# Kernel tuning notes

Hardware: AMD Instinct MI355X
Metric: run time of the kernel (lower is better)

## Reference

```python
import jax, jax.numpy as jnp
import numpy as np

B, T, D, H = 512, 1024, 64, 64     # batch, time, input_size, hidden_size
R = 4                              # number of reward heads
MH = 32                            # MLP hidden size


def setup_inputs() -> dict:
    key = jax.random.key(0)
    ks = jax.random.split(key, 16)
    s = lambda k, shape, scale=1.0: jax.random.normal(k, shape, dtype=jnp.float32) * scale
    inp = {
        "x": s(ks[0], (B, T, D)),
        # learned initial states (nn.Parameter randn(1,1,H) -> store as (H,))
        "h_init": s(ks[1], (H,)),
        "c_init": s(ks[2], (H,)),
        # LSTM params, PyTorch layout: W_ih (4H, D), W_hh (4H, H), gate order i,f,g,o
        "W_ih": s(ks[3], (4 * H, D), 1.0 / np.sqrt(H)),
        "W_hh": s(ks[4], (4 * H, H), 1.0 / np.sqrt(H)),
        "b_ih": s(ks[5], (4 * H,), 1.0 / np.sqrt(H)),
        "b_hh": s(ks[6], (4 * H,), 1.0 / np.sqrt(H)),
        # R stacked MLP heads: Linear(H,MH) -> ReLU -> Linear(MH,MH) -> ReLU -> Linear(MH,1)
        "W1": s(ks[7], (R, MH, H), 1.0 / np.sqrt(H)),
        "b1": s(ks[8], (R, MH), 1.0 / np.sqrt(H)),
        "W2": s(ks[9], (R, MH, MH), 1.0 / np.sqrt(MH)),
        "b2": s(ks[10], (R, MH), 1.0 / np.sqrt(MH)),
        "W3": s(ks[11], (R, 1, MH), 1.0 / np.sqrt(MH)),
        "b3": s(ks[12], (R, 1), 1.0 / np.sqrt(MH)),
    }
    return inp


def _lstm(x, h0, c0, W_ih, W_hh, b_ih, b_hh):
    # x: (B, T, D). Returns y: (B, T, H).
    Hh = h0.shape[-1]
    b = b_ih + b_hh                      # (4H,)
    # precompute input projections for all steps: (T, B, 4H)
    xg = jnp.einsum('btd,gd->tbg', x, W_ih) + b

    def step(carry, xg_t):
        h, c = carry                     # (B, H) each
        gates = xg_t + h @ W_hh.T        # (B, 4H)
        i, f, g, o = jnp.split(gates, 4, axis=-1)
        c = jax.nn.sigmoid(f) * c + jax.nn.sigmoid(i) * jnp.tanh(g)
        h = jax.nn.sigmoid(o) * jnp.tanh(c)
        return (h, c), h

    Bb = x.shape[0]
    h0b = jnp.broadcast_to(h0, (Bb, Hh))
    c0b = jnp.broadcast_to(c0, (Bb, Hh))
    _, ys = jax.lax.scan(step, (h0b, c0b), xg)   # ys: (T, B, H)
    return jnp.transpose(ys, (1, 0, 2))


def _heads(y, W1, b1, W2, b2, W3, b3):
    # y: (B, T, H) -> (R, B, T); all R heads computed in one batched einsum chain
    h1 = jax.nn.relu(jnp.einsum('bth,rmh->rbtm', y, W1) + b1[:, None, None, :])
    h2 = jax.nn.relu(jnp.einsum('rbtm,rnm->rbtn', h1, W2) + b2[:, None, None, :])
    out = jnp.einsum('rbtn,ron->rbto', h2, W3) + b3[:, None, None, :]
    return out[..., 0]                   # squeeze last dim -> (R, B, T)


def reference(x, h_init, c_init, W_ih, W_hh, b_ih, b_hh, W1, b1, W2, b2, W3, b3):
    y = _lstm(x, h_init, c_init, W_ih, W_hh, b_ih, b_hh)
    outs = _heads(y, W1, b1, W2, b2, W3, b3)   # (R, B, T); row r == rewards[r] head
    return (y, outs)
```

## Files before the change

kernel.cpp:

```cpp
#include <hip/hip_runtime.h>

#define BB 512
#define TT 1024
#define DD 64
#define HH 64
#define G4 256
#define RR 4
#define MHH 32
#define BT (BB * TT)
#define Y_SIZE (BB * TT * HH)

typedef _Float16 half8 __attribute__((ext_vector_type(8)));
typedef _Float16 half4 __attribute__((ext_vector_type(4)));
typedef float f32x4 __attribute__((ext_vector_type(4)));

#define MFMA16(a, b, c) __builtin_amdgcn_mfma_f32_16x16x32_f16((a), (b), (c), 0, 0, 0)

__device__ __forceinline__ float sigm(float x) {
    return __builtin_amdgcn_rcpf(1.0f + __expf(-x));
}
__device__ __forceinline__ float tanh_(float x) {
    return 1.0f - 2.0f * __builtin_amdgcn_rcpf(1.0f + __expf(2.0f * x));
}

__device__ __forceinline__ half8 cvt8(f32x4 a, f32x4 b) {
    half8 h;
    h[0] = (_Float16)a[0]; h[1] = (_Float16)a[1];
    h[2] = (_Float16)a[2]; h[3] = (_Float16)a[3];
    h[4] = (_Float16)b[0]; h[5] = (_Float16)b[1];
    h[6] = (_Float16)b[2]; h[7] = (_Float16)b[3];
    return h;
}

__global__ __launch_bounds__(256) void lstm_kernel(
    const float* __restrict__ x, const float* __restrict__ h_init,
    const float* __restrict__ c_init, const float* __restrict__ W_ih,
    const float* __restrict__ W_hh, const float* __restrict__ b_ih,
    const float* __restrict__ b_hh, float* __restrict__ y)
{
    __shared__ alignas(16) _Float16 xch[2][16][2][DD];
    __shared__ alignas(16) _Float16 hst[2][2][HH];

    const int tid  = threadIdx.x;
    const int wave = tid >> 6;
    const int lane = tid & 63;
    const int col  = lane & 15;
    const int quad = lane >> 4;
    const int sel  = (lane >> 3) & 1;
    const int r_act = lane >> 5;
    const int j    = (wave << 4) + col;
    const bool writer = ((lane >> 4) & 1) == 0;

    const int b0 = blockIdx.x * 2;

    half8 bf[4][4];
    float bias[4];
#pragma unroll
    for (int G = 0; G < 4; ++G) {
        const int n = (G << 6) + j;
        bias[G] = b_ih[n] + b_hh[n];
#pragma unroll
        for (int c = 0; c < 4; ++c) {
            const float* src = (c < 2) ? (W_ih + n * DD + c * 32 + quad * 8)
                                       : (W_hh + n * HH + (c - 2) * 32 + quad * 8);
            f32x4 w0 = *(const f32x4*)src;
            f32x4 w1 = *(const f32x4*)(src + 4);
            bf[G][c] = cvt8(w0, w1);
        }
    }

    float c_state = c_init[j];

    if (tid < 128) {
        const int rr = tid >> 6, jj = tid & 63;
        hst[0][rr][jj] = (_Float16)h_init[jj];
    }
    {
        const int ss = tid >> 4, rr = (tid >> 3) & 1, j0 = (tid & 7) << 3;
        const float* src = x + ((b0 + rr) * TT + ss) * DD + j0;
        f32x4 g0 = *(const f32x4*)src;
        f32x4 g1 = *(const f32x4*)(src + 4);
        *(half8*)&xch[0][ss][rr][j0] = cvt8(g0, g1);
    }
    __syncthreads();

    const int ss_pf = tid >> 4, rr_pf = (tid >> 3) & 1, j0_pf = (tid & 7) << 3;

    for (int ci = 0; ci < 64; ++ci) {
        const int buf = ci & 1;
        const bool pf = (ci + 1) < 64;
        f32x4 g0, g1;
        if (pf) {
            const float* src = x + ((b0 + rr_pf) * TT + ((ci + 1) << 4) + ss_pf) * DD + j0_pf;
            g0 = *(const f32x4*)src;
            g1 = *(const f32x4*)(src + 4);
        }
#pragma unroll
        for (int s = 0; s < 16; ++s) {
            const int t = (ci << 4) + s;
            const int p = s & 1;
            const _Float16* xrow = &xch[buf][s][sel][0];
            half8 a0 = *(const half8*)(xrow + quad * 8);
            half8 a1 = *(const half8*)(xrow + 32 + quad * 8);
            const _Float16* hrow = &hst[p][sel][0];
            half8 a2 = *(const half8*)(hrow + quad * 8);
            half8 a3 = *(const half8*)(hrow + 32 + quad * 8);

            f32x4 acc0 = {bias[0], bias[0], bias[0], bias[0]};
            f32x4 acc1 = {bias[1], bias[1], bias[1], bias[1]};
            f32x4 acc2 = {bias[2], bias[2], bias[2], bias[2]};
            f32x4 acc3 = {bias[3], bias[3], bias[3], bias[3]};
            acc0 = MFMA16(a0, bf[0][0], acc0); acc0 = MFMA16(a1, bf[0][1], acc0);
            acc0 = MFMA16(a2, bf[0][2], acc0); acc0 = MFMA16(a3, bf[0][3], acc0);
            acc1 = MFMA16(a0, bf[1][0], acc1); acc1 = MFMA16(a1, bf[1][1], acc1);
            acc1 = MFMA16(a2, bf[1][2], acc1); acc1 = MFMA16(a3, bf[1][3], acc1);
            acc2 = MFMA16(a0, bf[2][0], acc2); acc2 = MFMA16(a1, bf[2][1], acc2);
            acc2 = MFMA16(a2, bf[2][2], acc2); acc2 = MFMA16(a3, bf[2][3], acc2);
            acc3 = MFMA16(a0, bf[3][0], acc3); acc3 = MFMA16(a1, bf[3][1], acc3);
            acc3 = MFMA16(a2, bf[3][2], acc3); acc3 = MFMA16(a3, bf[3][3], acc3);

            const float si = sigm(acc0[0]);
            const float sf = sigm(acc1[0]);
            const float tg = tanh_(acc2[0]);
            const float so = sigm(acc3[0]);
            c_state = sf * c_state + si * tg;
            const float hv = so * tanh_(c_state);
            if (writer) {
                hst[p ^ 1][r_act][j] = (_Float16)hv;
                y[((b0 + r_act) * TT + t) * HH + j] = hv;
            }
            if (s == 15 && pf) {
                *(half8*)&xch[buf ^ 1][ss_pf][rr_pf][j0_pf] = cvt8(g0, g1);
            }
            __syncthreads();
        }
    }
}

__global__ __launch_bounds__(256) void heads_kernel(
    const float* __restrict__ y,
    const float* __restrict__ W1, const float* __restrict__ b1,
    const float* __restrict__ W2, const float* __restrict__ b2,
    const float* __restrict__ W3, const float* __restrict__ b3,
    float* __restrict__ outs)
{
    __shared__ alignas(16) _Float16 ybuf[64][72];
    __shared__ alignas(16) _Float16 h1buf[64][136];
    __shared__ alignas(16) _Float16 h2buf[64][136];

    const int tid  = threadIdx.x;
    const int wave = tid >> 6;
    const int lane = tid & 63;
    const int col  = lane & 15;
    const int quad = lane >> 4;
    const int arow = (wave << 4) + col;

    half8 w1f[8][2]; float bias1[8];
#pragma unroll
    for (int nt = 0; nt < 8; ++nt) {
        const int n = nt * 16 + col;
        bias1[nt] = b1[n];
#pragma unroll
        for (int c = 0; c < 2; ++c) {
            const float* src = W1 + n * 64 + c * 32 + quad * 8;
            w1f[nt][c] = cvt8(*(const f32x4*)src, *(const f32x4*)(src + 4));
        }
    }
    half8 w2f[8]; float bias2[8];
#pragma unroll
    for (int nt = 0; nt < 8; ++nt) {
        const int n = nt * 16 + col;
        bias2[nt] = b2[n];
        const float* src = W2 + n * 32 + quad * 8;
        w2f[nt] = cvt8(*(const f32x4*)src, *(const f32x4*)(src + 4));
    }
    const int hd3 = tid >> 6, row3 = tid & 63;
    float w3r[32];
#pragma unroll
    for (int i = 0; i < 32; i += 4) {
        f32x4 v = *(const f32x4*)(W3 + hd3 * 32 + i);
        w3r[i] = v[0]; w3r[i + 1] = v[1]; w3r[i + 2] = v[2]; w3r[i + 3] = v[3];
    }
    const float b3v = b3[hd3];

    for (int st = 0; st < 4; ++st) {
        const long base_row = (long)blockIdx.x * 256 + st * 64;
#pragma unroll
        for (int jj = 0; jj < 4; ++jj) {
            const int off = (jj * 256 + tid) * 4;
            const int row = off >> 6, cc = off & 63;
            f32x4 v = *(const f32x4*)(y + base_row * 64 + off);
            half4 hv = {(_Float16)v[0], (_Float16)v[1], (_Float16)v[2], (_Float16)v[3]};
            *(half4*)&ybuf[row][cc] = hv;
        }
        __syncthreads();

        half8 a0 = *(const half8*)&ybuf[arow][quad * 8];
        half8 a1 = *(const half8*)&ybuf[arow][32 + quad * 8];
#pragma unroll
        for (int nt = 0; nt < 8; ++nt) {
            f32x4 acc = {bias1[nt], bias1[nt], bias1[nt], bias1[nt]};
            acc = MFMA16(a0, w1f[nt][0], acc);
            acc = MFMA16(a1, w1f[nt][1], acc);
#pragma unroll
            for (int r = 0; r < 4; ++r) {
                float v = acc[r] > 0.0f ? acc[r] : 0.0f;
                h1buf[(wave << 4) + (quad << 2) + r][nt * 16 + col] = (_Float16)v;
            }
        }
        __syncthreads();

        half8 ah[4];
#pragma unroll
        for (int hd = 0; hd < 4; ++hd)
            ah[hd] = *(const half8*)&h1buf[arow][hd * 32 + quad * 8];
#pragma unroll
        for (int nt = 0; nt < 8; ++nt) {
            f32x4 acc = {bias2[nt], bias2[nt], bias2[nt], bias2[nt]};
            acc = MFMA16(ah[nt >> 1], w2f[nt], acc);
#pragma unroll
            for (int r = 0; r < 4; ++r) {
                float v = acc[r] > 0.0f ? acc[r] : 0.0f;
                h2buf[(wave << 4) + (quad << 2) + r][nt * 16 + col] = (_Float16)v;
            }
        }
        __syncthreads();

        float acc = b3v;
#pragma unroll
        for (int c = 0; c < 4; ++c) {
            half8 v = *(const half8*)&h2buf[row3][hd3 * 32 + c * 8];
#pragma unroll
            for (int u = 0; u < 8; ++u)
                acc = fmaf((float)v[u], w3r[c * 8 + u], acc);
        }
        outs[(long)hd3 * BT + base_row + row3] = acc;
        __syncthreads();
    }
}

extern "C" void kernel_launch(void* const* d_in, const int* in_sizes, int n_in,
                              void* d_out, int out_size, void* d_ws, size_t ws_size,
                              hipStream_t stream) {
    (void)in_sizes; (void)n_in; (void)out_size; (void)d_ws; (void)ws_size;
    const float* x      = (const float*)d_in[0];
    const float* h_init = (const float*)d_in[1];
    const float* c_init = (const float*)d_in[2];
    const float* W_ih   = (const float*)d_in[3];
    const float* W_hh   = (const float*)d_in[4];
    const float* b_ih   = (const float*)d_in[5];
    const float* b_hh   = (const float*)d_in[6];
    const float* W1     = (const float*)d_in[7];
    const float* b1     = (const float*)d_in[8];
    const float* W2     = (const float*)d_in[9];
    const float* b2     = (const float*)d_in[10];
    const float* W3     = (const float*)d_in[11];
    const float* b3     = (const float*)d_in[12];
    float* y    = (float*)d_out;
    float* outs = y + Y_SIZE;

    lstm_kernel<<<dim3(256), dim3(256), 0, stream>>>(x, h_init, c_init, W_ih, W_hh,
                                                     b_ih, b_hh, y);
    heads_kernel<<<dim3(2048), dim3(256), 0, stream>>>(y, W1, b1, W2, b2, W3, b3, outs);
}
```

Baseline: 570.5 us.

## Fuse MLP reward heads into LSTM kernel per 16-step chunk

The separate heads kernel is removed and its three MLP layers run inside the LSTM kernel after each 16-timestep chunk. Each chunk's hidden states are staged in shared memory, written to y with coalesced vector stores, and fed straight to MFMA head computation. This avoids re-reading y from global memory and a second launch. The cost is extra work on the serial recurrence path for each chunk. The x prefetch for the next chunk also moves from being in flight during the chunk to a synchronous load at the chunk boundary, which may expose load latency.

```diff
diff --git a/kernel.cpp b/kernel.cpp
--- a/kernel.cpp
+++ b/kernel.cpp
@@ -4,14 +4,12 @@
 #define TT 1024
 #define DD 64
 #define HH 64
-#define G4 256
 #define RR 4
 #define MHH 32
 #define BT (BB * TT)
 #define Y_SIZE (BB * TT * HH)
 
 typedef _Float16 half8 __attribute__((ext_vector_type(8)));
-typedef _Float16 half4 __attribute__((ext_vector_type(4)));
 typedef float f32x4 __attribute__((ext_vector_type(4)));
 
 #define MFMA16(a, b, c) __builtin_amdgcn_mfma_f32_16x16x32_f16((a), (b), (c), 0, 0, 0)
@@ -22,7 +20,6 @@
 __device__ __forceinline__ float tanh_(float x) {
     return 1.0f - 2.0f * __builtin_amdgcn_rcpf(1.0f + __expf(2.0f * x));
 }
-
 __device__ __forceinline__ half8 cvt8(f32x4 a, f32x4 b) {
     half8 h;
     h[0] = (_Float16)a[0]; h[1] = (_Float16)a[1];
@@ -32,14 +29,22 @@
     return h;
 }
 
-__global__ __launch_bounds__(256) void lstm_kernel(
+__global__ __launch_bounds__(256) void lstm_fused_kernel(
     const float* __restrict__ x, const float* __restrict__ h_init,
     const float* __restrict__ c_init, const float* __restrict__ W_ih,
     const float* __restrict__ W_hh, const float* __restrict__ b_ih,
-    const float* __restrict__ b_hh, float* __restrict__ y)
+    const float* __restrict__ b_hh,
+    const float* __restrict__ W1, const float* __restrict__ b1,
+    const float* __restrict__ W2, const float* __restrict__ b2,
+    const float* __restrict__ W3, const float* __restrict__ b3,
+    float* __restrict__ y, float* __restrict__ outs)
 {
     __shared__ alignas(16) _Float16 xch[2][16][2][DD];
     __shared__ alignas(16) _Float16 hst[2][2][HH];
+    __shared__ alignas(16) float    ybuf[2][16][68];
+    __shared__ alignas(16) _Float16 h1b[4][16][72];
+    __shared__ alignas(16) _Float16 h2b[4][16][72];
+    __shared__ alignas(16) float    w3s[128];
 
     const int tid  = threadIdx.x;
     const int wave = tid >> 6;
@@ -63,11 +68,36 @@
         for (int c = 0; c < 4; ++c) {
             const float* src = (c < 2) ? (W_ih + n * DD + c * 32 + quad * 8)
                                        : (W_hh + n * HH + (c - 2) * 32 + quad * 8);
-            f32x4 w0 = *(const f32x4*)src;
-            f32x4 w1 = *(const f32x4*)(src + 4);
-            bf[G][c] = cvt8(w0, w1);
-        }
-    }
+            bf[G][c] = cvt8(*(const f32x4*)src, *(const f32x4*)(src + 4));
+        }
+    }
+
+    const int pair = wave >> 1;
+    const int r_h  = wave & 1;
+    half8 w1f[4][2]; float bias1[4];
+#pragma unroll
+    for (int i = 0; i < 4; ++i) {
+        const int n1 = pair * 64 + i * 16 + col;
+        bias1[i] = b1[n1];
+#pragma unroll
+        for (int c = 0; c < 2; ++c) {
+            const float* src = W1 + n1 * 64 + c * 32 + quad * 8;
+            w1f[i][c] = cvt8(*(const f32x4*)src, *(const f32x4*)(src + 4));
+        }
+    }
+    half8 w2f[2][2]; float bias2[2][2];
+#pragma unroll
+    for (int hl = 0; hl < 2; ++hl)
+#pragma unroll
+        for (int i2 = 0; i2 < 2; ++i2) {
+            const int n2 = (pair * 2 + hl) * 32 + i2 * 16 + col;
+            bias2[hl][i2] = b2[n2];
+            const float* src = W2 + n2 * 32 + quad * 8;
+            w2f[hl][i2] = cvt8(*(const f32x4*)src, *(const f32x4*)(src + 4));
+        }
+    if (tid < 128) w3s[tid] = W3[tid];
+    const int g_l3 = pair * 2 + ((lane >> 4) & 1);
+    const float b3v = b3[g_l3];
 
     float c_state = c_init[j];
 
@@ -75,36 +105,25 @@
         const int rr = tid >> 6, jj = tid & 63;
         hst[0][rr][jj] = (_Float16)h_init[jj];
     }
+    const int ss_ld = tid >> 4, rr_ld = (tid >> 3) & 1, j0_ld = (tid & 7) << 3;
     {
-        const int ss = tid >> 4, rr = (tid >> 3) & 1, j0 = (tid & 7) << 3;
-        const float* src = x + ((b0 + rr) * TT + ss) * DD + j0;
-        f32x4 g0 = *(const f32x4*)src;
-        f32x4 g1 = *(const f32x4*)(src + 4);
-        *(half8*)&xch[0][ss][rr][j0] = cvt8(g0, g1);
+        const float* src = x + ((b0 + rr_ld) * TT + ss_ld) * DD + j0_ld;
+        *(half8*)&xch[0][ss_ld][rr_ld][j0_ld] =
+            cvt8(*(const f32x4*)src, *(const f32x4*)(src + 4));
     }
     __syncthreads();
-
-    const int ss_pf = tid >> 4, rr_pf = (tid >> 3) & 1, j0_pf = (tid & 7) << 3;
 
     for (int ci = 0; ci < 64; ++ci) {
         const int buf = ci & 1;
-        const bool pf = (ci + 1) < 64;
-        f32x4 g0, g1;
-        if (pf) {
-            const float* src = x + ((b0 + rr_pf) * TT + ((ci + 1) << 4) + ss_pf) * DD + j0_pf;
-            g0 = *(const f32x4*)src;
-            g1 = *(const f32x4*)(src + 4);
-        }
 #pragma unroll
         for (int s = 0; s < 16; ++s) {
-            const int t = (ci << 4) + s;
             const int p = s & 1;
+            const _Float16* hrow = &hst[p][sel][0];
+            half8 a2 = *(const half8*)(hrow + quad * 8);
+            half8 a3 = *(const half8*)(hrow + 32 + quad * 8);
             const _Float16* xrow = &xch[buf][s][sel][0];
             half8 a0 = *(const half8*)(xrow + quad * 8);
             half8 a1 = *(const half8*)(xrow + 32 + quad * 8);
-            const _Float16* hrow = &hst[p][sel][0];
-            half8 a2 = *(const half8*)(hrow + quad * 8);
-            half8 a3 = *(const half8*)(hrow + 32 + quad * 8);
 
             f32x4 acc0 = {bias[0], bias[0], bias[0], bias[0]};
             f32x4 acc1 = {bias[1], bias[1], bias[1], bias[1]};
@@ -127,114 +146,81 @@
             const float hv = so * tanh_(c_state);
             if (writer) {
                 hst[p ^ 1][r_act][j] = (_Float16)hv;
-                y[((b0 + r_act) * TT + t) * HH + j] = hv;
-            }
-            if (s == 15 && pf) {
-                *(half8*)&xch[buf ^ 1][ss_pf][rr_pf][j0_pf] = cvt8(g0, g1);
+                ybuf[r_act][s][j] = hv;
             }
             __syncthreads();
         }
-    }
-}
-
-__global__ __launch_bounds__(256) void heads_kernel(
-    const float* __restrict__ y,
-    const float* __restrict__ W1, const float* __restrict__ b1,
-    const float* __restrict__ W2, const float* __restrict__ b2,
-    const float* __restrict__ W3, const float* __restrict__ b3,
-    float* __restrict__ outs)
-{
-    __shared__ alignas(16) _Float16 ybuf[64][72];
-    __shared__ alignas(16) _Float16 h1buf[64][136];
-    __shared__ alignas(16) _Float16 h2buf[64][136];
-
-    const int tid  = threadIdx.x;
-    const int wave = tid >> 6;
-    const int lane = tid & 63;
-    const int col  = lane & 15;
-    const int quad = lane >> 4;
-    const int arow = (wave << 4) + col;
-
-    half8 w1f[8][2]; float bias1[8];
-#pragma unroll
-    for (int nt = 0; nt < 8; ++nt) {
-        const int n = nt * 16 + col;
-        bias1[nt] = b1[n];
-#pragma unroll
-        for (int c = 0; c < 2; ++c) {
-            const float* src = W1 + n * 64 + c * 32 + quad * 8;
-            w1f[nt][c] = cvt8(*(const f32x4*)src, *(const f32x4*)(src + 4));
-        }
-    }
-    half8 w2f[8]; float bias2[8];
-#pragma unroll
-    for (int nt = 0; nt < 8; ++nt) {
-        const int n = nt * 16 + col;
-        bias2[nt] = b2[n];
-        const float* src = W2 + n * 32 + quad * 8;
-        w2f[nt] = cvt8(*(const f32x4*)src, *(const f32x4*)(src + 4));
-    }
-    const int hd3 = tid >> 6, row3 = tid & 63;
-    float w3r[32];
-#pragma unroll
-    for (int i = 0; i < 32; i += 4) {
-        f32x4 v = *(const f32x4*)(W3 + hd3 * 32 + i);
-        w3r[i] = v[0]; w3r[i + 1] = v[1]; w3r[i + 2] = v[2]; w3r[i + 3] = v[3];
-    }
-    const float b3v = b3[hd3];
-
-    for (int st = 0; st < 4; ++st) {
-        const long base_row = (long)blockIdx.x * 256 + st * 64;
-#pragma unroll
-        for (int jj = 0; jj < 4; ++jj) {
-            const int off = (jj * 256 + tid) * 4;
-            const int row = off >> 6, cc = off & 63;
-            f32x4 v = *(const f32x4*)(y + base_row * 64 + off);
-            half4 hv = {(_Float16)v[0], (_Float16)v[1], (_Float16)v[2], (_Float16)v[3]};
-            *(half4*)&ybuf[row][cc] = hv;
-        }
-        __syncthreads();
-
-        half8 a0 = *(const half8*)&ybuf[arow][quad * 8];
-        half8 a1 = *(const half8*)&ybuf[arow][32 + quad * 8];
-#pragma unroll
-        for (int nt = 0; nt < 8; ++nt) {
-            f32x4 acc = {bias1[nt], bias1[nt], bias1[nt], bias1[nt]};
-            acc = MFMA16(a0, w1f[nt][0], acc);
-            acc = MFMA16(a1, w1f[nt][1], acc);
-#pragma unroll
-            for (int r = 0; r < 4; ++r) {
-                float v = acc[r] > 0.0f ? acc[r] : 0.0f;
-                h1buf[(wave << 4) + (quad << 2) + r][nt * 16 + col] = (_Float16)v;
+
+        {
+            const int r = tid >> 7, s = (tid >> 3) & 15, j0 = (tid & 7) << 3;
+            f32x4 v0 = *(const f32x4*)&ybuf[r][s][j0];
+            f32x4 v1 = *(const f32x4*)&ybuf[r][s][j0 + 4];
+            float* dst = y + (((long)(b0 + r) * TT + (ci << 4) + s) << 6) + j0;
+            *(f32x4*)dst = v0;
+            *(f32x4*)(dst + 4) = v1;
+        }
+        if (ci + 1 < 64) {
+            const float* src =
+                x + ((b0 + rr_ld) * TT + ((ci + 1) << 4) + ss_ld) * DD + j0_ld;
+            *(half8*)&xch[buf ^ 1][ss_ld][rr_ld][j0_ld] =
+                cvt8(*(const f32x4*)src, *(const f32x4*)(src + 4));
+        }
+        {
+            const int sr = lane & 15;
+            const float* yb = &ybuf[r_h][sr][0];
+            half8 a0 = cvt8(*(const f32x4*)(yb + quad * 8),
+                            *(const f32x4*)(yb + quad * 8 + 4));
+            half8 a1 = cvt8(*(const f32x4*)(yb + 32 + quad * 8),
+                            *(const f32x4*)(yb + 32 + quad * 8 + 4));
+#pragma unroll
+            for (int i = 0; i < 4; ++i) {
+                f32x4 acc = {bias1[i], bias1[i], bias1[i], bias1[i]};
+                acc = MFMA16(a0, w1f[i][0], acc);
+                acc = MFMA16(a1, w1f[i][1], acc);
+#pragma unroll
+                for (int r = 0; r < 4; ++r) {
+                    float v = acc[r] > 0.0f ? acc[r] : 0.0f;
+                    h1b[wave][(quad << 2) + r][i * 16 + col] = (_Float16)v;
+                }
             }
-        }
-        __syncthreads();
-
-        half8 ah[4];
-#pragma unroll
-        for (int hd = 0; hd < 4; ++hd)
-            ah[hd] = *(const half8*)&h1buf[arow][hd * 32 + quad * 8];
-#pragma unroll
-        for (int nt = 0; nt < 8; ++nt) {
-            f32x4 acc = {bias2[nt], bias2[nt], bias2[nt], bias2[nt]};
-            acc = MFMA16(ah[nt >> 1], w2f[nt], acc);
-#pragma unroll
-            for (int r = 0; r < 4; ++r) {
-                float v = acc[r] > 0.0f ? acc[r] : 0.0f;
-                h2buf[(wave << 4) + (quad << 2) + r][nt * 16 + col] = (_Float16)v;
+            half8 ah[2];
+#pragma unroll
+            for (int hl = 0; hl < 2; ++hl)
+                ah[hl] = *(const half8*)&h1b[wave][sr][hl * 32 + quad * 8];
+#pragma unroll
+            for (int hl = 0; hl < 2; ++hl)
+#pragma unroll
+                for (int i2 = 0; i2 < 2; ++i2) {
+                    f32x4 acc = {bias2[hl][i2], bias2[hl][i2],
+                                 bias2[hl][i2], bias2[hl][i2]};
+                    acc = MFMA16(ah[hl], w2f[hl][i2], acc);
+#pragma unroll
+                    for (int r = 0; r < 4; ++r) {
+                        float v = acc[r] > 0.0f ? acc[r] : 0.0f;
+                        h2b[wave][(quad << 2) + r][hl * 32 + i2 * 16 + col] =
+                            (_Float16)v;
+                    }
+                }
+            if (lane < 32) {
+                const int row = lane & 15, hl = lane >> 4;
+                float acc = b3v;
+#pragma unroll
+                for (int c4 = 0; c4 < 4; ++c4) {
+                    half8 v = *(const half8*)&h2b[wave][row][hl * 32 + c4 * 8];
+                    f32x4 w0 = *(const f32x4*)&w3s[g_l3 * 32 + c4 * 8];
+                    f32x4 w1v = *(const f32x4*)&w3s[g_l3 * 32 + c4 * 8 + 4];
+                    acc = fmaf((float)v[0], w0[0], acc);
+                    acc = fmaf((float)v[1], w0[1], acc);
+                    acc = fmaf((float)v[2], w0[2], acc);
+                    acc = fmaf((float)v[3], w0[3], acc);
+                    acc = fmaf((float)v[4], w1v[0], acc);
+                    acc = fmaf((float)v[5], w1v[1], acc);
+                    acc = fmaf((float)v[6], w1v[2], acc);
+                    acc = fmaf((float)v[7], w1v[3], acc);
+                }
+                outs[(long)g_l3 * BT + (long)(b0 + r_h) * TT + (ci << 4) + row] = acc;
             }
         }
-        __syncthreads();
-
-        float acc = b3v;
-#pragma unroll
-        for (int c = 0; c < 4; ++c) {
-            half8 v = *(const half8*)&h2buf[row3][hd3 * 32 + c * 8];
-#pragma unroll
-            for (int u = 0; u < 8; ++u)
-                acc = fmaf((float)v[u], w3r[c * 8 + u], acc);
-        }
-        outs[(long)hd3 * BT + base_row + row3] = acc;
         __syncthreads();
     }
 }
@@ -259,7 +245,7 @@
     float* y    = (float*)d_out;
     float* outs = y + Y_SIZE;
 
-    lstm_kernel<<<dim3(256), dim3(256), 0, stream>>>(x, h_init, c_init, W_ih, W_hh,
-                                                     b_ih, b_hh, y);
-    heads_kernel<<<dim3(2048), dim3(256), 0, stream>>>(y, W1, b1, W2, b2, W3, b3, outs);
-}
+    lstm_fused_kernel<<<dim3(256), dim3(256), 0, stream>>>(
+        x, h_init, c_init, W_ih, W_hh, b_ih, b_hh,
+        W1, b1, W2, b2, W3, b3, y, outs);
+}
```

Result: slower. 586.9 us (+2.9%).
